# Kernel tuning notes

Measured on AMD Instinct MI355X. Metric: run time of the kernel, lower is better.

The kernel has to match this reference:

```python
import jax, jax.numpy as jnp
import numpy as np

N_ENT = 100000
N_REL = 500
IN_DIM = 128
OUT_DIM = 128
E = 500000


def setup_inputs() -> dict:
    key = jax.random.key(0)
    ks = jax.random.split(key, 9)
    src = jax.random.randint(ks[0], (E,), 0, N_ENT)
    dst = jax.random.randint(ks[1], (E,), 0, N_ENT)
    rel = jax.random.randint(ks[2], (E,), 0, N_REL)
    ent_embed = jax.random.normal(ks[3], (N_ENT, IN_DIM), dtype=jnp.float32)
    rel_embed = jax.random.normal(ks[4], (N_REL, IN_DIM), dtype=jnp.float32)
    # xavier_normal with gain 1.414 for linear weights
    g = 1.414
    a_w = jax.random.normal(ks[5], (OUT_DIM, 3 * IN_DIM), dtype=jnp.float32) * (g * np.sqrt(2.0 / (3 * IN_DIM + OUT_DIM)))
    a_b = jnp.zeros((OUT_DIM,), dtype=jnp.float32)
    a2_w = jax.random.normal(ks[6], (1, OUT_DIM), dtype=jnp.float32) * (g * np.sqrt(2.0 / (OUT_DIM + 1)))
    a2_b = jnp.zeros((1,), dtype=jnp.float32)
    return {"ent_embed": ent_embed, "rel_embed": rel_embed, "a_w": a_w, "a_b": a_b,
            "a2_w": a2_w, "a2_b": a2_b, "src": src, "dst": dst, "rel": rel}


def reference(ent_embed, rel_embed, a_w, a_b, a2_w, a2_b, src, dst, rel):
    # gather: [E, 3*in_dim]
    h = jnp.concatenate([ent_embed[src], ent_embed[dst], rel_embed[rel]], axis=1)
    c = h @ a_w.T + a_b                      # [E, out_dim]
    b = jax.nn.leaky_relu(c @ a2_w.T + a2_b, negative_slope=0.01)  # [E, 1]
    e_b = jnp.exp(b)                          # [E, 1]
    temp1 = e_b * c                           # [E, out_dim]
    # scatter-sum into source nodes (SpecialSpmmFinal keyed on edges[0] = src)
    e_b_sum = jax.ops.segment_sum(e_b, src, num_segments=N_ENT)   # [N, 1]
    h_sum = jax.ops.segment_sum(temp1, src, num_segments=N_ENT)   # [N, out_dim]
    ebs = jnp.where(e_b_sum == 0, jnp.float32(1e-12), e_b_sum)
    h_ent = h_sum / ebs
    # scatter-mean of temp1 by relation id
    rel_sum = jax.ops.segment_sum(temp1, rel, num_segments=N_REL)          # [R, out_dim]
    rel_cnt = jax.ops.segment_sum(jnp.ones((temp1.shape[0],), jnp.float32), rel, num_segments=N_REL)
    h_rel = rel_sum / jnp.maximum(rel_cnt, 1.0)[:, None]
    return (jax.nn.elu(h_ent), jax.nn.elu(h_rel))
```

## Files before the change

### kernel.cpp

```cpp
#include <hip/hip_runtime.h>
#include <hip/hip_bf16.h>

#define N_ENT_C 100000
#define N_REL_C 500
#define NEDGE_C 500000
#define SCAN_BLOCKS 391
#define EPB 1024
#define NB_EDGE 489
#define CHUNK_B 62
#define MT_TOTAL 6250
#define ENT_GRID 1250

#define OFF_WTHI  0
#define OFF_WTLO  16384
#define OFF_WTR   32768
#define OFF_PR    49152
#define OFF_PRH   113152
#define OFF_STAGE 145152
#define OFF_PSH   1445760
#define OFF_PDH   7845760

#define DO_OSRC     0
#define DO_DSTS     100000
#define DO_RELS     600000
#define DO_QS       1100000
#define DO_QD       1200000
#define DO_QR       1300000
#define SCRATCH_ROWS 10161
#define DO_HSRC     1300512
#define DO_BSUM     1400512
#define DO_RELSTART 1401024
#define DO_PART8    1401536
#define DO_CHUNKOFF 1405632
#define DO_BLKHIST  1409728
#define DO_BLKOFFS  1660096
#define DO_SRCR     1910464
#define DO_DSTR     2410464
#define DO_RELP     2910464

typedef short bf16x8 __attribute__((ext_vector_type(8)));
typedef float f32x4  __attribute__((ext_vector_type(4)));
typedef unsigned short u16x8 __attribute__((ext_vector_type(8)));

__device__ inline unsigned short bf_rne(float x) {
    unsigned int u = __float_as_uint(x);
    u += 0x7FFF + ((u >> 16) & 1);
    return (unsigned short)(u >> 16);
}
__device__ inline float bf2f(unsigned short h) {
    return __uint_as_float(((unsigned int)h) << 16);
}

__global__ void prep_w(const float* __restrict__ aw, unsigned short* __restrict__ Wthi,
                       unsigned short* __restrict__ Wtlo, float* __restrict__ Wtr) {
    int idx = blockIdx.x * 256 + threadIdx.x;
    if (idx < 32768) {
        int n = idx >> 7, k = idx & 127;
        float v = (n < 128) ? aw[n * 384 + k] : aw[(n - 128) * 384 + 128 + k];
        unsigned short h = bf_rne(v);
        Wthi[idx] = h;
        Wtlo[idx] = bf_rne(v - bf2f(h));
    } else if (idx < 49152) {
        int t = idx - 32768;
        int k = t >> 7, o = t & 127;
        Wtr[t] = aw[o * 384 + 256 + k];
    }
}

__global__ void rel_proj(const float* __restrict__ rele, const float* __restrict__ Wtr,
                         const float* __restrict__ ab, const float* __restrict__ a2w,
                         float* __restrict__ Pr, unsigned short* __restrict__ PrH,
                         float* __restrict__ qr) {
    int r = blockIdx.x;
    int o = threadIdx.x;
    float acc = ab[o];
    for (int k = 0; k < 128; ++k)
        acc = fmaf(rele[r * 128 + k], Wtr[k * 128 + o], acc);
    Pr[r * 128 + o] = acc;
    PrH[r * 128 + o] = bf_rne(acc);
    __shared__ float red[128];
    red[o] = acc * a2w[o];
    __syncthreads();
    for (int off = 64; off > 0; off >>= 1) {
        if (o < off) red[o] += red[o + off];
        __syncthreads();
    }
    if (o == 0) qr[r] = red[0];
}

__global__ __launch_bounds__(256, 2) void ent_mfma(const float* __restrict__ ent,
                                                   const unsigned short* __restrict__ Wthi,
                                                   const unsigned short* __restrict__ Wtlo,
                                                   const float* __restrict__ a2w,
                                                   unsigned short* __restrict__ PsH,
                                                   unsigned short* __restrict__ PdH,
                                                   float* __restrict__ qs,
                                                   float* __restrict__ qd) {
    const int tid = threadIdx.x;
    const int w = tid >> 6, lane = tid & 63;
    const int l15 = lane & 15, lh = lane >> 4;
    const int n0 = w * 64;

    bf16x8 wh[4][4], wl[4][4];
#pragma unroll
    for (int nf = 0; nf < 4; ++nf) {
        int n = n0 + nf * 16 + l15;
#pragma unroll
        for (int ks = 0; ks < 4; ++ks) {
            int kb = ks * 32 + lh * 8;
            wh[nf][ks] = *(const bf16x8*)(Wthi + n * 128 + kb);
            wl[nf][ks] = *(const bf16x8*)(Wtlo + n * 128 + kb);
        }
    }
    float a2v[4][4];
#pragma unroll
    for (int nf = 0; nf < 4; ++nf)
#pragma unroll
        for (int v = 0; v < 4; ++v)
            a2v[nf][v] = a2w[(n0 + nf * 16 + lh * 4 + v) & 127];

    const bool isPs = (w < 2);
    unsigned short* PH = isPs ? PsH : PdH;
    float* qout = isPs ? qs : qd;
    const int colbase0 = (n0 & 127) + lh * 4;

    f32x4 zz = {0.f, 0.f, 0.f, 0.f};

    for (int mt = blockIdx.x; mt < MT_TOTAL; mt += ENT_GRID) {
        const int m = mt * 16 + l15;
        bf16x8 eh[4], el[4];
#pragma unroll
        for (int ks = 0; ks < 4; ++ks) {
            int kb = ks * 32 + lh * 8;
            float4 e0 = *(const float4*)&ent[(size_t)m * 128 + kb];
            float4 e1 = *(const float4*)&ent[(size_t)m * 128 + kb + 4];
            float f[8] = {e0.x, e0.y, e0.z, e0.w, e1.x, e1.y, e1.z, e1.w};
            bf16x8 hv, lv;
#pragma unroll
            for (int j = 0; j < 8; ++j) {
                unsigned short h = bf_rne(f[j]);
                hv[j] = (short)h;
                lv[j] = (short)bf_rne(f[j] - bf2f(h));
            }
            eh[ks] = hv; el[ks] = lv;
        }

        f32x4 acc[4];
#pragma unroll
        for (int nf = 0; nf < 4; ++nf) acc[nf] = zz;
#pragma unroll
        for (int ks = 0; ks < 4; ++ks)
#pragma unroll
            for (int nf = 0; nf < 4; ++nf) {
                acc[nf] = __builtin_amdgcn_mfma_f32_16x16x32_bf16(wh[nf][ks], eh[ks], acc[nf], 0, 0, 0);
                acc[nf] = __builtin_amdgcn_mfma_f32_16x16x32_bf16(wh[nf][ks], el[ks], acc[nf], 0, 0, 0);
                acc[nf] = __builtin_amdgcn_mfma_f32_16x16x32_bf16(wl[nf][ks], eh[ks], acc[nf], 0, 0, 0);
            }

        float qp = 0.f;
#pragma unroll
        for (int nf = 0; nf < 4; ++nf) {
            ushort4 st;
            st.x = bf_rne(acc[nf][0]);
            st.y = bf_rne(acc[nf][1]);
            st.z = bf_rne(acc[nf][2]);
            st.w = bf_rne(acc[nf][3]);
#pragma unroll
            for (int v = 0; v < 4; ++v) qp = fmaf(acc[nf][v], a2v[nf][v], qp);
            *(ushort4*)&PH[(size_t)m * 128 + colbase0 + nf * 16] = st;
        }
        qp += __shfl_xor(qp, 16);
        qp += __shfl_xor(qp, 32);
        if (lane < 16) unsafeAtomicAdd(&qout[m], qp);
    }
}

__global__ __launch_bounds__(256) void edge_hist(const int* __restrict__ src,
                                                 const int* __restrict__ rel,
                                                 int* __restrict__ histSrc,
                                                 int* __restrict__ blkHist) {
    __shared__ int lh[512];
    int tid = threadIdx.x;
    lh[tid] = 0; lh[tid + 256] = 0;
    __syncthreads();
    int base = blockIdx.x * EPB;
#pragma unroll
    for (int j = 0; j < 4; ++j) {
        int e = base + j * 256 + tid;
        if (e < NEDGE_C) {
            atomicAdd(&histSrc[src[e]], 1);
            atomicAdd(&lh[rel[e]], 1);
        }
    }
    __syncthreads();
    blkHist[blockIdx.x * 512 + tid] = lh[tid];
    blkHist[blockIdx.x * 512 + 256 + tid] = lh[tid + 256];
}

__global__ void colsum(const int* __restrict__ blkHist, int* __restrict__ partial) {
    int r = threadIdx.x;
    int k = blockIdx.x;
    int b0 = k * CHUNK_B;
    int b1 = min(b0 + CHUNK_B, NB_EDGE);
    int t = 0;
    for (int b = b0; b < b1; ++b) t += blkHist[b * 512 + r];
    partial[k * 512 + r] = t;
}

__global__ void scan512(const int* __restrict__ partial, int* __restrict__ relStart,
                        int* __restrict__ chunkOff) {
    __shared__ int a[512], b2[512];
    int tid = threadIdx.x;
    int p8[8];
    int t = 0;
#pragma unroll
    for (int k = 0; k < 8; ++k) { p8[k] = partial[k * 512 + tid]; t += p8[k]; }
    a[tid] = t;
    __syncthreads();
    int v = t;
    int* cur = a; int* nxt = b2;
    for (int off = 1; off < 512; off <<= 1) {
        int x = cur[tid] + ((tid >= off) ? cur[tid - off] : 0);
        nxt[tid] = x;
        __syncthreads();
        int* tmp = cur; cur = nxt; nxt = tmp;
    }
    int excl = cur[tid] - v;
    relStart[tid] = excl;
    int run = excl;
#pragma unroll
    for (int k = 0; k < 8; ++k) { chunkOff[k * 512 + tid] = run; run += p8[k]; }
}

__global__ void colscan(const int* __restrict__ blkHist, const int* __restrict__ chunkOff,
                        int* __restrict__ blockOffs) {
    int r = threadIdx.x;
    int k = blockIdx.x;
    int b0 = k * CHUNK_B;
    int b1 = min(b0 + CHUNK_B, NB_EDGE);
    int off = chunkOff[k * 512 + r];
    for (int b = b0; b < b1; ++b) {
        blockOffs[b * 512 + r] = off;
        off += blkHist[b * 512 + r];
    }
}

__global__ void scan_blockred(const int* __restrict__ hist, int* __restrict__ blockSums, int n) {
    __shared__ int s[256];
    int tid = threadIdx.x;
    int i = blockIdx.x * 256 + tid;
    s[tid] = (i < n) ? hist[i] : 0;
    __syncthreads();
    for (int off = 128; off > 0; off >>= 1) {
        if (tid < off) s[tid] += s[tid + off];
        __syncthreads();
    }
    if (tid == 0) blockSums[blockIdx.x] = s[0];
}

__global__ void scan_single(int* __restrict__ data, int n) {
    __shared__ int a[1024], b2[1024];
    int tid = threadIdx.x;
    int v = (tid < n) ? data[tid] : 0;
    a[tid] = v;
    __syncthreads();
    int* cur = a; int* nxt = b2;
    for (int off = 1; off < 1024; off <<= 1) {
        int x = cur[tid] + ((tid >= off) ? cur[tid - off] : 0);
        nxt[tid] = x;
        __syncthreads();
        int* t = cur; cur = nxt; nxt = t;
    }
    if (tid < n) data[tid] = cur[tid] - v;
}

__global__ void scan_final(const int* __restrict__ hist, const int* __restrict__ blockOffs,
                           int* __restrict__ offs, int n) {
    __shared__ int a[256], b2[256];
    int tid = threadIdx.x;
    int i = blockIdx.x * 256 + tid;
    int v = (i < n) ? hist[i] : 0;
    a[tid] = v;
    __syncthreads();
    int* cur = a; int* nxt = b2;
    for (int off = 1; off < 256; off <<= 1) {
        int x = cur[tid] + ((tid >= off) ? cur[tid - off] : 0);
        nxt[tid] = x;
        __syncthreads();
        int* t = cur; cur = nxt; nxt = t;
    }
    if (i < n) offs[i] = cur[tid] - v + blockOffs[blockIdx.x];
}

__global__ __launch_bounds__(256) void scatter_both(const int* __restrict__ src,
                                                    const int* __restrict__ dst,
                                                    const int* __restrict__ rel,
                                                    int* __restrict__ offsSrc,
                                                    const int* __restrict__ blockOffs,
                                                    int* __restrict__ dstS, int* __restrict__ relS,
                                                    int* __restrict__ srcR, int* __restrict__ dstR) {
    __shared__ int lh[512];
    int tid = threadIdx.x;
    lh[tid] = 0; lh[tid + 256] = 0;
    __syncthreads();
    int base = blockIdx.x * EPB;
    const int* bo = &blockOffs[blockIdx.x * 512];
#pragma unroll
    for (int j = 0; j < 4; ++j) {
        int e = base + j * 256 + tid;
        if (e < NEDGE_C) {
            int s = src[e], d = dst[e], r = rel[e];
            int p = atomicAdd(&offsSrc[s], 1);
            dstS[p] = d; relS[p] = r;
            int lr = atomicAdd(&lh[r], 1);
            int q = bo[r] + lr;
            srcR[q] = s; dstR[q] = d;
        }
    }
}

__global__ __launch_bounds__(256) void rel_phase(const unsigned short* __restrict__ PsH,
                                                 const unsigned short* __restrict__ PdH,
                                                 const float* __restrict__ qs,
                                                 const float* __restrict__ qd,
                                                 const float* __restrict__ qr,
                                                 const int* __restrict__ relStart,
                                                 const int* __restrict__ srcR,
                                                 const int* __restrict__ dstR,
                                                 const float* __restrict__ a2b,
                                                 float* __restrict__ relpart) {
    int r = blockIdx.x >> 3;
    int p = blockIdx.x & 7;
    int start = relStart[r];
    int end = relStart[r + 1];
    int tid = threadIdx.x;
    int w = tid >> 6;
    int h = (tid >> 5) & 1;
    int l = tid & 31;
    int slot = p * 8 + w * 2 + h;
    float bb = a2b[0];
    float qrr = qr[r];
    float4 acc = make_float4(0.f, 0.f, 0.f, 0.f);
    float ebs = 0.f;
    for (int i = start + slot; i < end; i += 64) {
        int s = srcR[i], d = dstR[i];
        float b = qs[s] + qd[d] + qrr + bb;
        b = (b > 0.f) ? b : 0.01f * b;
        float eb = expf(b);
        ushort4 pv = *(const ushort4*)&PsH[(size_t)s * 128 + l * 4];
        ushort4 dv = *(const ushort4*)&PdH[(size_t)d * 128 + l * 4];
        acc.x = fmaf(eb, bf2f(pv.x) + bf2f(dv.x), acc.x);
        acc.y = fmaf(eb, bf2f(pv.y) + bf2f(dv.y), acc.y);
        acc.z = fmaf(eb, bf2f(pv.z) + bf2f(dv.z), acc.z);
        acc.w = fmaf(eb, bf2f(pv.w) + bf2f(dv.w), acc.w);
        ebs += eb;
    }
    __shared__ float vred[8][128];
    __shared__ float sred[8];
    int sub = w * 2 + h;
    *(float4*)&vred[sub][l * 4] = acc;
    if (l == 0) sred[sub] = ebs;
    __syncthreads();
    if (tid < 128) {
        float v = 0.f;
#pragma unroll
        for (int k2 = 0; k2 < 8; ++k2) v += vred[k2][tid];
        float e = 0.f;
#pragma unroll
        for (int k2 = 0; k2 < 8; ++k2) e += sred[k2];
        int pi = r * 8 + p;
        relpart[pi * 132 + tid] = v;
        if (tid == 0) relpart[pi * 132 + 128] = e;
    }
}

__global__ void rel_fin(const float* __restrict__ relpart, const float* __restrict__ Pr,
                        const int* __restrict__ relStart, float* __restrict__ outRel) {
    int r = blockIdx.x;
    int o = threadIdx.x;
    float v = 0.f, e = 0.f;
#pragma unroll
    for (int p = 0; p < 8; ++p) {
        v += relpart[(r * 8 + p) * 132 + o];
        e += relpart[(r * 8 + p) * 132 + 128];
    }
    float cnt = (float)(relStart[r + 1] - relStart[r]);
    float h = (v + e * Pr[r * 128 + o]) / fmaxf(cnt, 1.f);
    outRel[r * 128 + o] = (h > 0.f) ? h : (expf(h) - 1.f);
}

__global__ __launch_bounds__(256) void src_phase(const unsigned short* __restrict__ PsH,
                                                 const unsigned short* __restrict__ PdH,
                                                 const unsigned short* __restrict__ PrH,
                                                 const float* __restrict__ qs,
                                                 const float* __restrict__ qd,
                                                 const float* __restrict__ qr,
                                                 const int* __restrict__ offsSrc,
                                                 const int* __restrict__ dstS,
                                                 const int* __restrict__ relS,
                                                 const float* __restrict__ a2b,
                                                 float* __restrict__ stage,
                                                 float* __restrict__ out) {
    int wid = (blockIdx.x * 256 + threadIdx.x) >> 6;
    if (wid >= N_ENT_C) return;
    int lane = threadIdx.x & 63;
    int g = lane >> 4, l = lane & 15;
    int s = wid;
    int start = (s == 0) ? 0 : offsSrc[s - 1];
    int end = offsSrc[s];
    float* dstp = (s < SCRATCH_ROWS) ? &stage[(size_t)s * 128] : &out[(size_t)s * 128];
    if (end == start) {
        if (g == 0) {
            *(float4*)&dstp[l * 8] = make_float4(0.f, 0.f, 0.f, 0.f);
            *(float4*)&dstp[l * 8 + 4] = make_float4(0.f, 0.f, 0.f, 0.f);
        }
        return;
    }
    float bb = a2b[0];
    float qss = qs[s];
    float acc[8];
#pragma unroll
    for (int j = 0; j < 8; ++j) acc[j] = 0.f;
    float ebs = 0.f;
    for (int i = start + g; i < end; i += 4) {
        int d = dstS[i], r = relS[i];
        float b = qss + qd[d] + qr[r] + bb;
        b = (b > 0.f) ? b : 0.01f * b;
        float eb = expf(b);
        u16x8 dv = *(const u16x8*)&PdH[(size_t)d * 128 + l * 8];
        u16x8 rv = *(const u16x8*)&PrH[(size_t)r * 128 + l * 8];
#pragma unroll
        for (int j = 0; j < 8; ++j)
            acc[j] = fmaf(eb, bf2f(dv[j]) + bf2f(rv[j]), acc[j]);
        ebs += eb;
    }
#pragma unroll
    for (int j = 0; j < 8; ++j) {
        acc[j] += __shfl_xor(acc[j], 16);
        acc[j] += __shfl_xor(acc[j], 32);
    }
    ebs += __shfl_xor(ebs, 16);
    ebs += __shfl_xor(ebs, 32);
    if (g == 0) {
        float inv = 1.f / ebs;
        u16x8 ps = *(const u16x8*)&PsH[(size_t)s * 128 + l * 8];
        float h[8];
#pragma unroll
        for (int j = 0; j < 8; ++j) {
            float x = bf2f(ps[j]) + acc[j] * inv;
            h[j] = (x > 0.f) ? x : (expf(x) - 1.f);
        }
        *(float4*)&dstp[l * 8]     = make_float4(h[0], h[1], h[2], h[3]);
        *(float4*)&dstp[l * 8 + 4] = make_float4(h[4], h[5], h[6], h[7]);
    }
}

extern "C" void kernel_launch(void* const* d_in, const int* in_sizes, int n_in,
                              void* d_out, int out_size, void* d_ws, size_t ws_size,
                              hipStream_t stream) {
    const float* ent  = (const float*)d_in[0];
    const float* rele = (const float*)d_in[1];
    const float* aw   = (const float*)d_in[2];
    const float* ab   = (const float*)d_in[3];
    const float* a2w  = (const float*)d_in[4];
    const float* a2b  = (const float*)d_in[5];
    const int* src    = (const int*)d_in[6];
    const int* dst    = (const int*)d_in[7];
    const int* rel    = (const int*)d_in[8];
    float* out = (float*)d_out;

    float* ws = (float*)d_ws;
    unsigned short* Wthi = (unsigned short*)(ws + OFF_WTHI);
    unsigned short* Wtlo = (unsigned short*)(ws + OFF_WTLO);
    float* Wtr = ws + OFF_WTR;
    float* Pr  = ws + OFF_PR;
    unsigned short* PrH = (unsigned short*)(ws + OFF_PRH);
    float* stage = ws + OFF_STAGE;
    unsigned short* PsH = (unsigned short*)(ws + OFF_PSH);
    unsigned short* PdH = (unsigned short*)(ws + OFF_PDH);

    int* dI = (int*)d_out;
    int* offsSrc  = dI + DO_OSRC;
    int* dstS     = dI + DO_DSTS;
    int* relS     = dI + DO_RELS;
    float* qs     = (float*)dI + DO_QS;
    float* qd     = (float*)dI + DO_QD;
    float* qr     = (float*)dI + DO_QR;
    int* histSrc  = dI + DO_HSRC;
    int* bsum     = dI + DO_BSUM;
    int* relStart = dI + DO_RELSTART;
    int* part8    = dI + DO_PART8;
    int* chunkOff = dI + DO_CHUNKOFF;
    int* blkHist  = dI + DO_BLKHIST;
    int* blockOffs= dI + DO_BLKOFFS;
    int* srcR     = dI + DO_SRCR;
    int* dstR     = dI + DO_DSTR;
    float* relpart = (float*)dI + DO_RELP;

    hipMemsetAsync(dI + DO_QS, 0, (size_t)(DO_HSRC + N_ENT_C - DO_QS) * sizeof(int), stream);

    prep_w<<<192, 256, 0, stream>>>(aw, Wthi, Wtlo, Wtr);
    rel_proj<<<N_REL_C, 128, 0, stream>>>(rele, Wtr, ab, a2w, Pr, PrH, qr);
    ent_mfma<<<ENT_GRID, 256, 0, stream>>>(ent, Wthi, Wtlo, a2w, PsH, PdH, qs, qd);

    edge_hist<<<NB_EDGE, 256, 0, stream>>>(src, rel, histSrc, blkHist);
    colsum<<<8, 512, 0, stream>>>(blkHist, part8);
    scan512<<<1, 512, 0, stream>>>(part8, relStart, chunkOff);
    colscan<<<8, 512, 0, stream>>>(blkHist, chunkOff, blockOffs);
    scan_blockred<<<SCAN_BLOCKS, 256, 0, stream>>>(histSrc, bsum, N_ENT_C);
    scan_single<<<1, 1024, 0, stream>>>(bsum, SCAN_BLOCKS);
    scan_final<<<SCAN_BLOCKS, 256, 0, stream>>>(histSrc, bsum, offsSrc, N_ENT_C);
    scatter_both<<<NB_EDGE, 256, 0, stream>>>(src, dst, rel, offsSrc, blockOffs,
                                              dstS, relS, srcR, dstR);

    rel_phase<<<N_REL_C * 8, 256, 0, stream>>>(PsH, PdH, qs, qd, qr, relStart, srcR, dstR,
                                               a2b, relpart);
    rel_fin<<<N_REL_C, 128, 0, stream>>>(relpart, Pr, relStart, out + (size_t)N_ENT_C * 128);

    src_phase<<<(N_ENT_C + 3) / 4, 256, 0, stream>>>(PsH, PdH, PrH, qs, qd, qr,
                                                     offsSrc, dstS, relS, a2b, stage, out);

    hipMemcpyAsync(out, stage, (size_t)SCRATCH_ROWS * 128 * sizeof(float),
                   hipMemcpyDeviceToDevice, stream);
}
```

Measured before the change: 265.5 us.

## Split entity bf16 conversion into separate pass and restructure MFMA projection kernel

```diff
diff --git a/kernel.cpp b/kernel.cpp
--- a/kernel.cpp
+++ b/kernel.cpp
@@ -9,34 +9,34 @@
 #define NB_EDGE 489
 #define CHUNK_B 62
 #define MT_TOTAL 6250
-#define ENT_GRID 1250
+#define MT_PER_BLOCK 8
+#define MFMA_GRID 782
+#define CVT_GRID 1563
 
 #define OFF_WTHI  0
 #define OFF_WTLO  16384
 #define OFF_WTR   32768
 #define OFF_PR    49152
 #define OFF_PRH   113152
-#define OFF_STAGE 145152
-#define OFF_PSH   1445760
-#define OFF_PDH   7845760
-
-#define DO_OSRC     0
-#define DO_DSTS     100000
-#define DO_RELS     600000
-#define DO_QS       1100000
-#define DO_QD       1200000
-#define DO_QR       1300000
-#define SCRATCH_ROWS 10161
-#define DO_HSRC     1300512
-#define DO_BSUM     1400512
-#define DO_RELSTART 1401024
-#define DO_PART8    1401536
-#define DO_CHUNKOFF 1405632
-#define DO_BLKHIST  1409728
-#define DO_BLKOFFS  1660096
-#define DO_SRCR     1910464
-#define DO_DSTR     2410464
-#define DO_RELP     2910464
+#define OFF_QR    145920
+#define OFF_QS    146432
+#define OFF_QD    246432
+#define OFF_OSRC  346432
+#define OFF_DSTS  446432
+#define OFF_RELS  946432
+#define OFF_PSH   1446432
+#define OFF_PDH   7846432
+
+#define DO_HSRC     0
+#define DO_BSUM     100000
+#define DO_RELSTART 100512
+#define DO_PART8    101024
+#define DO_CHUNKOFF 105120
+#define DO_BLKHIST  109216
+#define DO_BLKOFFS  359584
+#define DO_SRCR     609952
+#define DO_DSTR     1109952
+#define DO_RELP     1609952
 
 typedef short bf16x8 __attribute__((ext_vector_type(8)));
 typedef float f32x4  __attribute__((ext_vector_type(4)));
@@ -88,22 +88,49 @@
     if (o == 0) qr[r] = red[0];
 }
 
-__global__ __launch_bounds__(256, 2) void ent_mfma(const float* __restrict__ ent,
-                                                   const unsigned short* __restrict__ Wthi,
-                                                   const unsigned short* __restrict__ Wtlo,
-                                                   const float* __restrict__ a2w,
-                                                   unsigned short* __restrict__ PsH,
-                                                   unsigned short* __restrict__ PdH,
-                                                   float* __restrict__ qs,
-                                                   float* __restrict__ qd) {
+__global__ __launch_bounds__(256) void ent_cvt(const float* __restrict__ ent,
+                                               uint4* __restrict__ EntF) {
+    int gw = blockIdx.x * 256 + threadIdx.x;
+    int mt = gw >> 6;
+    if (mt >= MT_TOTAL) return;
+    int lane = gw & 63;
+    int row = mt * 16 + (lane & 15);
+    int kb0 = (lane >> 4) * 8;
+    const float* rp = ent + (size_t)row * 128;
+    size_t mb = (size_t)mt * 8;
+#pragma unroll
+    for (int ks = 0; ks < 4; ++ks) {
+        float4 a = *(const float4*)(rp + ks * 32 + kb0);
+        float4 b = *(const float4*)(rp + ks * 32 + kb0 + 4);
+        float f[8] = {a.x, a.y, a.z, a.w, b.x, b.y, b.z, b.w};
+        union { unsigned short u[8]; uint4 v; } H, L;
+#pragma unroll
+        for (int j = 0; j < 8; ++j) {
+            unsigned short h = bf_rne(f[j]);
+            H.u[j] = h;
+            L.u[j] = bf_rne(f[j] - bf2f(h));
+        }
+        EntF[(mb + ks) * 64 + lane] = H.v;
+        EntF[(mb + 4 + ks) * 64 + lane] = L.v;
+    }
+}
+
+__global__ __launch_bounds__(512, 4) void ent_mfma3(const uint4* __restrict__ EntF,
+                                                    const unsigned short* __restrict__ Wthi,
+                                                    const unsigned short* __restrict__ Wtlo,
+                                                    const float* __restrict__ a2w,
+                                                    unsigned short* __restrict__ PsH,
+                                                    unsigned short* __restrict__ PdH,
+                                                    float* __restrict__ qs,
+                                                    float* __restrict__ qd) {
     const int tid = threadIdx.x;
     const int w = tid >> 6, lane = tid & 63;
     const int l15 = lane & 15, lh = lane >> 4;
-    const int n0 = w * 64;
-
-    bf16x8 wh[4][4], wl[4][4];
-#pragma unroll
-    for (int nf = 0; nf < 4; ++nf) {
+    const int n0 = w * 32;
+
+    bf16x8 wh[2][4], wl[2][4];
+#pragma unroll
+    for (int nf = 0; nf < 2; ++nf) {
         int n = n0 + nf * 16 + l15;
 #pragma unroll
         for (int ks = 0; ks < 4; ++ks) {
@@ -112,54 +139,56 @@
             wl[nf][ks] = *(const bf16x8*)(Wtlo + n * 128 + kb);
         }
     }
-    float a2v[4][4];
-#pragma unroll
-    for (int nf = 0; nf < 4; ++nf)
+#pragma unroll
+    for (int nf = 0; nf < 2; ++nf)
+#pragma unroll
+        for (int ks = 0; ks < 4; ++ks) {
+            asm volatile("" : "+v"(wh[nf][ks]));
+            asm volatile("" : "+v"(wl[nf][ks]));
+        }
+
+    float a2v[2][4];
+#pragma unroll
+    for (int nf = 0; nf < 2; ++nf)
 #pragma unroll
         for (int v = 0; v < 4; ++v)
             a2v[nf][v] = a2w[(n0 + nf * 16 + lh * 4 + v) & 127];
 
-    const bool isPs = (w < 2);
+    const bool isPs = (w < 4);
     unsigned short* PH = isPs ? PsH : PdH;
     float* qout = isPs ? qs : qd;
-    const int colbase0 = (n0 & 127) + lh * 4;
-
+    const int colbase = (n0 & 127) + lh * 4;
+
+    const bf16x8* EB = (const bf16x8*)EntF;
     f32x4 zz = {0.f, 0.f, 0.f, 0.f};
-
-    for (int mt = blockIdx.x; mt < MT_TOTAL; mt += ENT_GRID) {
-        const int m = mt * 16 + l15;
+    const int mt0 = blockIdx.x * MT_PER_BLOCK;
+
+#pragma unroll
+    for (int i = 0; i < MT_PER_BLOCK; ++i) {
+        int mt = mt0 + i;
+        if (mt >= MT_TOTAL) break;
+        size_t mb = (size_t)mt * 512;
         bf16x8 eh[4], el[4];
 #pragma unroll
         for (int ks = 0; ks < 4; ++ks) {
-            int kb = ks * 32 + lh * 8;
-            float4 e0 = *(const float4*)&ent[(size_t)m * 128 + kb];
-            float4 e1 = *(const float4*)&ent[(size_t)m * 128 + kb + 4];
-            float f[8] = {e0.x, e0.y, e0.z, e0.w, e1.x, e1.y, e1.z, e1.w};
-            bf16x8 hv, lv;
-#pragma unroll
-            for (int j = 0; j < 8; ++j) {
-                unsigned short h = bf_rne(f[j]);
-                hv[j] = (short)h;
-                lv[j] = (short)bf_rne(f[j] - bf2f(h));
-            }
-            eh[ks] = hv; el[ks] = lv;
-        }
-
-        f32x4 acc[4];
-#pragma unroll
-        for (int nf = 0; nf < 4; ++nf) acc[nf] = zz;
+            eh[ks] = EB[mb + (size_t)ks * 64 + lane];
+            el[ks] = EB[mb + 256 + (size_t)ks * 64 + lane];
+        }
+        f32x4 acc[2];
+        acc[0] = zz; acc[1] = zz;
 #pragma unroll
         for (int ks = 0; ks < 4; ++ks)
 #pragma unroll
-            for (int nf = 0; nf < 4; ++nf) {
+            for (int nf = 0; nf < 2; ++nf) {
                 acc[nf] = __builtin_amdgcn_mfma_f32_16x16x32_bf16(wh[nf][ks], eh[ks], acc[nf], 0, 0, 0);
                 acc[nf] = __builtin_amdgcn_mfma_f32_16x16x32_bf16(wh[nf][ks], el[ks], acc[nf], 0, 0, 0);
                 acc[nf] = __builtin_amdgcn_mfma_f32_16x16x32_bf16(wl[nf][ks], eh[ks], acc[nf], 0, 0, 0);
             }
 
+        int m = mt * 16 + l15;
         float qp = 0.f;
 #pragma unroll
-        for (int nf = 0; nf < 4; ++nf) {
+        for (int nf = 0; nf < 2; ++nf) {
             ushort4 st;
             st.x = bf_rne(acc[nf][0]);
             st.y = bf_rne(acc[nf][1]);
@@ -167,7 +196,7 @@
             st.w = bf_rne(acc[nf][3]);
 #pragma unroll
             for (int v = 0; v < 4; ++v) qp = fmaf(acc[nf][v], a2v[nf][v], qp);
-            *(ushort4*)&PH[(size_t)m * 128 + colbase0 + nf * 16] = st;
+            *(ushort4*)&PH[(size_t)m * 128 + colbase + nf * 16] = st;
         }
         qp += __shfl_xor(qp, 16);
         qp += __shfl_xor(qp, 32);
@@ -399,7 +428,6 @@
                                                  const int* __restrict__ dstS,
                                                  const int* __restrict__ relS,
                                                  const float* __restrict__ a2b,
-                                                 float* __restrict__ stage,
                                                  float* __restrict__ out) {
     int wid = (blockIdx.x * 256 + threadIdx.x) >> 6;
     if (wid >= N_ENT_C) return;
@@ -408,7 +436,7 @@
     int s = wid;
     int start = (s == 0) ? 0 : offsSrc[s - 1];
     int end = offsSrc[s];
-    float* dstp = (s < SCRATCH_ROWS) ? &stage[(size_t)s * 128] : &out[(size_t)s * 128];
+    float* dstp = &out[(size_t)s * 128];
     if (end == start) {
         if (g == 0) {
             *(float4*)&dstp[l * 8] = make_float4(0.f, 0.f, 0.f, 0.f);
@@ -475,17 +503,17 @@
     float* Wtr = ws + OFF_WTR;
     float* Pr  = ws + OFF_PR;
     unsigned short* PrH = (unsigned short*)(ws + OFF_PRH);
-    float* stage = ws + OFF_STAGE;
+    float* qr  = ws + OFF_QR;
+    float* qs  = ws + OFF_QS;
+    float* qd  = ws + OFF_QD;
+    int* offsSrc = (int*)(ws + OFF_OSRC);
+    int* dstS    = (int*)(ws + OFF_DSTS);
+    int* relS    = (int*)(ws + OFF_RELS);
     unsigned short* PsH = (unsigned short*)(ws + OFF_PSH);
     unsigned short* PdH = (unsigned short*)(ws + OFF_PDH);
 
     int* dI = (int*)d_out;
-    int* offsSrc  = dI + DO_OSRC;
-    int* dstS     = dI + DO_DSTS;
-    int* relS     = dI + DO_RELS;
-    float* qs     = (float*)dI + DO_QS;
-    float* qd     = (float*)dI + DO_QD;
-    float* qr     = (float*)dI + DO_QR;
+    uint4* EntF   = (uint4*)d_out;
     int* histSrc  = dI + DO_HSRC;
     int* bsum     = dI + DO_BSUM;
     int* relStart = dI + DO_RELSTART;
@@ -497,12 +525,14 @@
     int* dstR     = dI + DO_DSTR;
     float* relpart = (float*)dI + DO_RELP;
 
-    hipMemsetAsync(dI + DO_QS, 0, (size_t)(DO_HSRC + N_ENT_C - DO_QS) * sizeof(int), stream);
+    hipMemsetAsync(ws + OFF_QR, 0, (size_t)(OFF_OSRC - OFF_QR) * sizeof(float), stream);
 
     prep_w<<<192, 256, 0, stream>>>(aw, Wthi, Wtlo, Wtr);
     rel_proj<<<N_REL_C, 128, 0, stream>>>(rele, Wtr, ab, a2w, Pr, PrH, qr);
-    ent_mfma<<<ENT_GRID, 256, 0, stream>>>(ent, Wthi, Wtlo, a2w, PsH, PdH, qs, qd);
-
+    ent_cvt<<<CVT_GRID, 256, 0, stream>>>(ent, EntF);
+    ent_mfma3<<<MFMA_GRID, 512, 0, stream>>>(EntF, Wthi, Wtlo, a2w, PsH, PdH, qs, qd);
+
+    hipMemsetAsync(histSrc, 0, (size_t)N_ENT_C * sizeof(int), stream);
     edge_hist<<<NB_EDGE, 256, 0, stream>>>(src, rel, histSrc, blkHist);
     colsum<<<8, 512, 0, stream>>>(blkHist, part8);
     scan512<<<1, 512, 0, stream>>>(part8, relStart, chunkOff);
@@ -518,8 +548,5 @@
     rel_fin<<<N_REL_C, 128, 0, stream>>>(relpart, Pr, relStart, out + (size_t)N_ENT_C * 128);
 
     src_phase<<<(N_ENT_C + 3) / 4, 256, 0, stream>>>(PsH, PdH, PrH, qs, qd, qr,
-                                                     offsSrc, dstS, relS, a2b, stage, out);
-
-    hipMemcpyAsync(out, stage, (size_t)SCRATCH_ROWS * 128 * sizeof(float),
-                   hipMemcpyDeviceToDevice, stream);
-}
+                                                     offsSrc, dstS, relS, a2b, out);
+}
```

Measured after the change: 273.5 us. 3.0% more time.
